# Optimization experiments

Measured on AMD Instinct MI355X. Metric: run time of the kernel, lower is better.

## Reference

```python
import jax, jax.numpy as jnp
import numpy as np

H = 512  # hidden_size; feature dim is 2H = 1024


def setup_inputs() -> dict:
    key = jax.random.key(0)
    ks = jax.random.split(key, 8)
    B, S, D2 = 32, 2048, 2 * H
    scale = 1.0 / np.sqrt(D2)
    return {
        "query": jax.random.normal(ks[0], (B, 4, H), dtype=jnp.float32),
        "keys": jax.random.normal(ks[1], (B, S, D2), dtype=jnp.float32),
        "Wa_w": jax.random.uniform(ks[2], (D2, D2), jnp.float32, -scale, scale),
        "Wa_b": jax.random.uniform(ks[3], (D2,), jnp.float32, -scale, scale),
        "Ua_w": jax.random.uniform(ks[4], (D2, D2), jnp.float32, -scale, scale),
        "Ua_b": jax.random.uniform(ks[5], (D2,), jnp.float32, -scale, scale),
        "Va_w": jax.random.uniform(ks[6], (1, D2), jnp.float32, -scale, scale),
        "Va_b": jax.random.uniform(ks[7], (1,), jnp.float32, -scale, scale),
    }


def reference(query, keys, Wa_w, Wa_b, Ua_w, Ua_b, Va_w, Va_b):
    B, D = query.shape[0], query.shape[-1]
    q = query.reshape(B, 2, -1, D)
    # last timestep of each direction, concatenated -> (B, 1, 2H)
    q = jnp.concatenate([q[:, 0, -1, :], q[:, 1, -1, :]], axis=-1)[:, None, :]
    # additive attention energies: (B, S, 2H)
    e = jnp.tanh((q @ Wa_w.T + Wa_b) + (keys @ Ua_w.T + Ua_b))
    scores = (e @ Va_w.T + Va_b)[..., 0][:, None, :]  # (B, 1, S)
    weights = jax.nn.softmax(scores, axis=-1)
    context = jnp.einsum("bqs,bsd->bqd", weights, keys)  # (B, 1, 2H)
    return context, weights
```

## Files before the change

### kernel.cpp

```cpp
#include <hip/hip_runtime.h>
#include <hip/hip_bf16.h>


typedef __attribute__((ext_vector_type(8))) short bf16x8;
typedef __attribute__((ext_vector_type(4))) float f32x4;

__device__ __forceinline__ unsigned pk_bf16(float x, float y) {
  union { __hip_bfloat162 h; unsigned u; } c;
  c.h = __float22bfloat162_rn(make_float2(x, y));
  return c.u;
}

__device__ __forceinline__ float fast_tanh(float x) {
  float e = __expf(2.0f * x);
  return 1.0f - 2.0f / (e + 1.0f);
}

typedef const __attribute__((address_space(1))) void* gas_t;
typedef __attribute__((address_space(3))) void* las_t;
__device__ __forceinline__ void ld_lds16(const void* g, void* l) {
  __builtin_amdgcn_global_load_lds((gas_t)g, (las_t)l, 16, 0, 0);
}

__global__ __launch_bounds__(256) void k_cvt_all(const float4* __restrict__ keys,
                                                 const float4* __restrict__ ua,
                                                 uint2* __restrict__ keys16,
                                                 uint2* __restrict__ ua16) {
  size_t i = (size_t)blockIdx.x * 256 + threadIdx.x;
  const float4* src;
  uint2* dst;
  size_t idx;
  if (i < 262144) { src = ua; dst = ua16; idx = i; }
  else            { src = keys; dst = keys16; idx = i - 262144; }
  float4 v = src[idx];
  uint2 o;
  o.x = pk_bf16(v.x, v.y);
  o.y = pk_bf16(v.z, v.w);
  dst[idx] = o;
}

__global__ __launch_bounds__(256) void k_qw(const float* __restrict__ query,
                                            const float* __restrict__ Wa_w,
                                            const float* __restrict__ Wa_b,
                                            const float* __restrict__ Ua_b,
                                            float* __restrict__ qW) {
  const int jc = blockIdx.x, b = blockIdx.y, t = threadIdx.x;
  __shared__ float4 qloc[256];
  {
    const float* base = (t < 128) ? (query + b * 2048 + 512) : (query + b * 2048 + 1536 - 512);
    qloc[t] = *(const float4*)(base + t * 4);
  }
  __syncthreads();
  const int jl = t >> 3, ks = t & 7;
  const int j = jc * 32 + jl;
  const float* wrow = Wa_w + j * 1024;
  float s = 0.f;
  #pragma unroll
  for (int i = 0; i < 32; ++i) {
    float4 wv = *(const float4*)(wrow + i * 32 + ks * 4);
    float4 q4 = qloc[i * 8 + ks];
    s += wv.x * q4.x + wv.y * q4.y + wv.z * q4.z + wv.w * q4.w;
  }
  s += __shfl_xor(s, 1);
  s += __shfl_xor(s, 2);
  s += __shfl_xor(s, 4);
  if (ks == 0) qW[b * 1024 + j] = s + Wa_b[j] + Ua_b[j];
}

__global__ __launch_bounds__(256) void k_score2(const unsigned short* __restrict__ keys16,
                                                const unsigned short* __restrict__ Uab,
                                                const float* __restrict__ qW,
                                                const float* __restrict__ Va,
                                                float* __restrict__ scores) {
  __shared__ __align__(16) unsigned short As[128 * 64];
  __shared__ __align__(16) unsigned short Bs[128 * 64];
  const int h = blockIdx.x;
  const int x = h & 7, g = h >> 3;
  const int jblk = g & 7;
  const int rblk = x + ((g >> 3) << 3);
  const int t = threadIdx.x;
  const int lane = t & 63, w = t >> 6;
  const int wm = w >> 1, wn = w & 1;
  const int l15 = lane & 15, quad = lane >> 4;
  const int row0 = rblk * 128, j0 = jblk * 128;
  const int lr = lane >> 3;
  const int sg = (lane & 7) ^ lr;

  f32x4 acc[4][4];
  #pragma unroll
  for (int i = 0; i < 4; i++)
    #pragma unroll
    for (int j = 0; j < 4; j++) acc[i][j] = (f32x4){0.f, 0.f, 0.f, 0.f};

  const int rb = l15 & 7;
  const int aoff = (wm * 64 + l15) * 64;
  const int boff = (wn * 64 + l15) * 64;

  const unsigned short* ga = keys16 + (size_t)(row0 + (w * 4) * 8 + lr) * 1024 + sg * 8;
  const unsigned short* gb = Uab + (size_t)(j0 + (w * 4) * 8 + lr) * 1024 + sg * 8;

  for (int k0 = 0; k0 < 1024; k0 += 64) {
    if (k0) __syncthreads();
    #pragma unroll
    for (int i = 0; i < 4; ++i) {
      const int c = w * 4 + i;
      ld_lds16(ga + (size_t)i * 8 * 1024 + k0, As + c * 512);
      ld_lds16(gb + (size_t)i * 8 * 1024 + k0, Bs + c * 512);
    }
    __syncthreads();
    #pragma unroll
    for (int ks = 0; ks < 2; ++ks) {
      const int xf = ((ks * 4 + quad) ^ rb) * 8;
      bf16x8 af[4], bfr[4];
      #pragma unroll
      for (int i = 0; i < 4; i++) af[i] = *(const bf16x8*)(As + aoff + i * 1024 + xf);
      #pragma unroll
      for (int i = 0; i < 4; i++) bfr[i] = *(const bf16x8*)(Bs + boff + i * 1024 + xf);
      #pragma unroll
      for (int i = 0; i < 4; i++)
        #pragma unroll
        for (int j = 0; j < 4; j++)
          acc[i][j] = __builtin_amdgcn_mfma_f32_16x16x32_bf16(af[i], bfr[j], acc[i][j], 0, 0, 0);
    }
  }

  const int b = row0 >> 11;
  float va[4], qb[4];
  #pragma unroll
  for (int j = 0; j < 4; j++) {
    int jg = j0 + wn * 64 + j * 16 + l15;
    va[j] = Va[jg];
    qb[j] = qW[b * 1024 + jg];
  }
  #pragma unroll
  for (int i = 0; i < 4; i++) {
    #pragma unroll
    for (int r = 0; r < 4; r++) {
      float s = 0.f;
      #pragma unroll
      for (int j = 0; j < 4; j++)
        s += va[j] * fast_tanh(acc[i][j][r] + qb[j]);
      s += __shfl_xor(s, 1);
      s += __shfl_xor(s, 2);
      s += __shfl_xor(s, 4);
      s += __shfl_xor(s, 8);
      if (l15 == 0) {
        int rg = row0 + wm * 64 + i * 16 + quad * 4 + r;
        atomicAdd(&scores[rg], s);
      }
    }
  }
}

__global__ __launch_bounds__(256) void k_score1(const float* __restrict__ keys,
                                                const unsigned short* __restrict__ Uab,
                                                const float* __restrict__ qW,
                                                const float* __restrict__ Va,
                                                float* __restrict__ scores) {
  __shared__ __align__(16) unsigned short As[128 * 72];
  __shared__ __align__(16) unsigned short Bs[128 * 72];
  const int jblk = blockIdx.x, rblk = blockIdx.y;
  const int t = threadIdx.x;
  const int lane = t & 63, w = t >> 6;
  const int wm = w >> 1, wn = w & 1;
  const int l15 = lane & 15, quad = lane >> 4;
  const int row0 = rblk * 128, j0 = jblk * 128;
  f32x4 acc[4][4];
  #pragma unroll
  for (int i = 0; i < 4; i++)
    #pragma unroll
    for (int j = 0; j < 4; j++) acc[i][j] = (f32x4){0.f, 0.f, 0.f, 0.f};
  for (int k0 = 0; k0 < 1024; k0 += 64) {
    __syncthreads();
    #pragma unroll
    for (int i = 0; i < 8; ++i) {
      int c = i * 256 + t, m = c >> 4, f4 = c & 15;
      float4 v = *(const float4*)(keys + (size_t)(row0 + m) * 1024 + k0 + f4 * 4);
      uint2 p;
      p.x = pk_bf16(v.x, v.y);
      p.y = pk_bf16(v.z, v.w);
      *(uint2*)(As + m * 72 + f4 * 4) = p;
    }
    #pragma unroll
    for (int i = 0; i < 4; ++i) {
      int c = i * 256 + t, j = c >> 3, k8 = c & 7;
      *(uint4*)(Bs + j * 72 + k8 * 8) = *(const uint4*)(Uab + (size_t)(j0 + j) * 1024 + k0 + k8 * 8);
    }
    __syncthreads();
    #pragma unroll
    for (int ks = 0; ks < 2; ++ks) {
      bf16x8 af[4], bfr[4];
      #pragma unroll
      for (int i = 0; i < 4; i++)
        af[i] = *(const bf16x8*)(As + (wm * 64 + i * 16 + l15) * 72 + ks * 32 + quad * 8);
      #pragma unroll
      for (int i = 0; i < 4; i++)
        bfr[i] = *(const bf16x8*)(Bs + (wn * 64 + i * 16 + l15) * 72 + ks * 32 + quad * 8);
      #pragma unroll
      for (int i = 0; i < 4; i++)
        #pragma unroll
        for (int j = 0; j < 4; j++)
          acc[i][j] = __builtin_amdgcn_mfma_f32_16x16x32_bf16(af[i], bfr[j], acc[i][j], 0, 0, 0);
    }
  }
  const int b = row0 >> 11;
  float va[4], qb[4];
  #pragma unroll
  for (int j = 0; j < 4; j++) {
    int jg = j0 + wn * 64 + j * 16 + l15;
    va[j] = Va[jg];
    qb[j] = qW[b * 1024 + jg];
  }
  #pragma unroll
  for (int i = 0; i < 4; i++)
    #pragma unroll
    for (int r = 0; r < 4; r++) {
      float s = 0.f;
      #pragma unroll
      for (int j = 0; j < 4; j++) s += va[j] * fast_tanh(acc[i][j][r] + qb[j]);
      s += __shfl_xor(s, 1);
      s += __shfl_xor(s, 2);
      s += __shfl_xor(s, 4);
      s += __shfl_xor(s, 8);
      if (l15 == 0) atomicAdd(&scores[row0 + wm * 64 + i * 16 + quad * 4 + r], s);
    }
}

__global__ __launch_bounds__(256) void k_softmax(const float* __restrict__ scores,
                                                 float* __restrict__ wout,
                                                 float* __restrict__ ctx) {
  const int b = blockIdx.x, t = threadIdx.x;
  const int lane = t & 63, w = t >> 6;
  *(float4*)(ctx + b * 1024 + t * 4) = (float4){0.f, 0.f, 0.f, 0.f};
  __shared__ float red[4];
  float v[8];
  float mx = -1e30f;
  #pragma unroll
  for (int i = 0; i < 8; i++) {
    v[i] = scores[b * 2048 + i * 256 + t];
    mx = fmaxf(mx, v[i]);
  }
  #pragma unroll
  for (int off = 1; off < 64; off <<= 1) mx = fmaxf(mx, __shfl_xor(mx, off));
  if (lane == 0) red[w] = mx;
  __syncthreads();
  mx = fmaxf(fmaxf(red[0], red[1]), fmaxf(red[2], red[3]));
  float sum = 0.f;
  #pragma unroll
  for (int i = 0; i < 8; i++) {
    v[i] = __expf(v[i] - mx);
    sum += v[i];
  }
  #pragma unroll
  for (int off = 1; off < 64; off <<= 1) sum += __shfl_xor(sum, off);
  __syncthreads();
  if (lane == 0) red[w] = sum;
  __syncthreads();
  sum = red[0] + red[1] + red[2] + red[3];
  float inv = 1.0f / sum;
  #pragma unroll
  for (int i = 0; i < 8; i++) wout[b * 2048 + i * 256 + t] = v[i] * inv;
}

__global__ __launch_bounds__(256) void k_context(const float* __restrict__ keys,
                                                 const float* __restrict__ wts,
                                                 float* __restrict__ ctx) {
  const int sc = blockIdx.x;
  const int b  = blockIdx.y;
  const int t  = threadIdx.x;
  __shared__ float wl[64];
  if (t < 64) wl[t] = wts[b * 2048 + sc * 64 + t];
  __syncthreads();
  const float4* kp = (const float4*)(keys + ((size_t)(b * 2048 + sc * 64) << 10)) + t;
  float4 a = {0.f, 0.f, 0.f, 0.f};
  #pragma unroll 8
  for (int s = 0; s < 64; ++s) {
    float4 kv = kp[s * 256];
    float wv = wl[s];
    a.x += wv * kv.x; a.y += wv * kv.y; a.z += wv * kv.z; a.w += wv * kv.w;
  }
  float* o = ctx + b * 1024 + t * 4;
  atomicAdd(o + 0, a.x);
  atomicAdd(o + 1, a.y);
  atomicAdd(o + 2, a.z);
  atomicAdd(o + 3, a.w);
}

extern "C" void kernel_launch(void* const* d_in, const int* in_sizes, int n_in,
                              void* d_out, int out_size, void* d_ws, size_t ws_size,
                              hipStream_t stream) {
  const float* query = (const float*)d_in[0];
  const float* keys  = (const float*)d_in[1];
  const float* Wa_w  = (const float*)d_in[2];
  const float* Wa_b  = (const float*)d_in[3];
  const float* Ua_w  = (const float*)d_in[4];
  const float* Ua_b  = (const float*)d_in[5];
  const float* Va_w  = (const float*)d_in[6];

  float* scores = (float*)d_ws;
  float* qW     = scores + 65536;
  unsigned short* Uab    = (unsigned short*)(qW + 32768);
  unsigned short* keys16 = Uab + 1024 * 1024;
  const size_t NEED_A = 2490368ull + 134217728ull;

  float* ctx = (float*)d_out;
  float* wts = ctx + 32768;

  hipMemsetAsync(scores, 0, 65536 * sizeof(float), stream);
  k_qw<<<dim3(32, 32), 256, 0, stream>>>(query, Wa_w, Wa_b, Ua_b, qW);

  if (ws_size >= NEED_A) {
    k_cvt_all<<<66560, 256, 0, stream>>>((const float4*)keys, (const float4*)Ua_w,
                                         (uint2*)keys16, (uint2*)Uab);
    k_score2<<<4096, 256, 0, stream>>>(keys16, Uab, qW, Va_w, scores);
  } else {
    k_cvt_all<<<1024, 256, 0, stream>>>((const float4*)keys, (const float4*)Ua_w,
                                        (uint2*)keys16, (uint2*)Uab);
    k_score1<<<dim3(8, 512), 256, 0, stream>>>(keys, Uab, qW, Va_w, scores);
  }

  k_softmax<<<32, 256, 0, stream>>>(scores, wts, ctx);
  k_context<<<dim3(32, 32), 256, 0, stream>>>(keys, wts, ctx);
}
```

Baseline: 591.9 us.

## Fuse prologue kernels and compute context from bf16 keys

Merges the scores memset, the query projection and the fp32-to-bf16 conversion into one launch to cut launch overhead. The context reduction now reads the bf16 copy of keys instead of fp32, halving the bytes read in that stage, and splits rows across two half-blocks with an LDS combine. The score GEMM gets an occupancy hint and a reordered fragment load loop to lower register pressure. Using bf16 keys for the context reduces output precision.

```diff
diff --git a/kernel.cpp b/kernel.cpp
--- a/kernel.cpp
+++ b/kernel.cpp
@@ -11,6 +11,12 @@
   return c.u;
 }
 
+__device__ __forceinline__ float bf2f(short u) {
+  union { unsigned u; float f; } c;
+  c.u = ((unsigned)(unsigned short)u) << 16;
+  return c.f;
+}
+
 __device__ __forceinline__ float fast_tanh(float x) {
   float e = __expf(2.0f * x);
   return 1.0f - 2.0f / (e + 1.0f);
@@ -22,29 +28,33 @@
   __builtin_amdgcn_global_load_lds((gas_t)g, (las_t)l, 16, 0, 0);
 }
 
-__global__ __launch_bounds__(256) void k_cvt_all(const float4* __restrict__ keys,
-                                                 const float4* __restrict__ ua,
-                                                 uint2* __restrict__ keys16,
-                                                 uint2* __restrict__ ua16) {
-  size_t i = (size_t)blockIdx.x * 256 + threadIdx.x;
-  const float4* src;
-  uint2* dst;
-  size_t idx;
-  if (i < 262144) { src = ua; dst = ua16; idx = i; }
-  else            { src = keys; dst = keys16; idx = i - 262144; }
-  float4 v = src[idx];
-  uint2 o;
-  o.x = pk_bf16(v.x, v.y);
-  o.y = pk_bf16(v.z, v.w);
-  dst[idx] = o;
-}
-
-__global__ __launch_bounds__(256) void k_qw(const float* __restrict__ query,
-                                            const float* __restrict__ Wa_w,
-                                            const float* __restrict__ Wa_b,
-                                            const float* __restrict__ Ua_b,
-                                            float* __restrict__ qW) {
-  const int jc = blockIdx.x, b = blockIdx.y, t = threadIdx.x;
+__global__ __launch_bounds__(256) void k_fused(const float* __restrict__ query,
+                                               const float* __restrict__ Wa_w,
+                                               const float* __restrict__ Wa_b,
+                                               const float* __restrict__ Ua_b,
+                                               const float4* __restrict__ keys,
+                                               const float4* __restrict__ ua,
+                                               float* __restrict__ qW,
+                                               uint2* __restrict__ keys16,
+                                               uint2* __restrict__ ua16,
+                                               float* __restrict__ scores) {
+  const int t = threadIdx.x;
+  if (blockIdx.x >= 1024) {
+    size_t i = (size_t)(blockIdx.x - 1024) * 256 + t;
+    const float4* src;
+    uint2* dst;
+    size_t idx;
+    if (i < 262144) { src = ua; dst = ua16; idx = i; }
+    else            { src = keys; dst = keys16; idx = i - 262144; }
+    float4 v = src[idx];
+    uint2 o;
+    o.x = pk_bf16(v.x, v.y);
+    o.y = pk_bf16(v.z, v.w);
+    dst[idx] = o;
+    return;
+  }
+  if (t < 64) scores[blockIdx.x * 64 + t] = 0.f;
+  const int jc = blockIdx.x >> 5, b = blockIdx.x & 31;
   __shared__ float4 qloc[256];
   {
     const float* base = (t < 128) ? (query + b * 2048 + 512) : (query + b * 2048 + 1536 - 512);
@@ -67,11 +77,11 @@
   if (ks == 0) qW[b * 1024 + j] = s + Wa_b[j] + Ua_b[j];
 }
 
-__global__ __launch_bounds__(256) void k_score2(const unsigned short* __restrict__ keys16,
-                                                const unsigned short* __restrict__ Uab,
-                                                const float* __restrict__ qW,
-                                                const float* __restrict__ Va,
-                                                float* __restrict__ scores) {
+__global__ __launch_bounds__(256, 4) void k_score2(const unsigned short* __restrict__ keys16,
+                                                   const unsigned short* __restrict__ Uab,
+                                                   const float* __restrict__ qW,
+                                                   const float* __restrict__ Va,
+                                                   float* __restrict__ scores) {
   __shared__ __align__(16) unsigned short As[128 * 64];
   __shared__ __align__(16) unsigned short Bs[128 * 64];
   const int h = blockIdx.x;
@@ -111,16 +121,18 @@
     #pragma unroll
     for (int ks = 0; ks < 2; ++ks) {
       const int xf = ((ks * 4 + quad) ^ rb) * 8;
-      bf16x8 af[4], bfr[4];
-      #pragma unroll
-      for (int i = 0; i < 4; i++) af[i] = *(const bf16x8*)(As + aoff + i * 1024 + xf);
-      #pragma unroll
-      for (int i = 0; i < 4; i++) bfr[i] = *(const bf16x8*)(Bs + boff + i * 1024 + xf);
-      #pragma unroll
-      for (int i = 0; i < 4; i++)
-        #pragma unroll
-        for (int j = 0; j < 4; j++)
-          acc[i][j] = __builtin_amdgcn_mfma_f32_16x16x32_bf16(af[i], bfr[j], acc[i][j], 0, 0, 0);
+      bf16x8 bfr0 = *(const bf16x8*)(Bs + boff + 0 * 1024 + xf);
+      bf16x8 bfr1 = *(const bf16x8*)(Bs + boff + 1 * 1024 + xf);
+      bf16x8 bfr2 = *(const bf16x8*)(Bs + boff + 2 * 1024 + xf);
+      bf16x8 bfr3 = *(const bf16x8*)(Bs + boff + 3 * 1024 + xf);
+      #pragma unroll
+      for (int i = 0; i < 4; i++) {
+        bf16x8 af = *(const bf16x8*)(As + aoff + i * 1024 + xf);
+        acc[i][0] = __builtin_amdgcn_mfma_f32_16x16x32_bf16(af, bfr0, acc[i][0], 0, 0, 0);
+        acc[i][1] = __builtin_amdgcn_mfma_f32_16x16x32_bf16(af, bfr1, acc[i][1], 0, 0, 0);
+        acc[i][2] = __builtin_amdgcn_mfma_f32_16x16x32_bf16(af, bfr2, acc[i][2], 0, 0, 0);
+        acc[i][3] = __builtin_amdgcn_mfma_f32_16x16x32_bf16(af, bfr3, acc[i][3], 0, 0, 0);
+      }
     }
   }
 
@@ -262,9 +274,41 @@
   for (int i = 0; i < 8; i++) wout[b * 2048 + i * 256 + t] = v[i] * inv;
 }
 
-__global__ __launch_bounds__(256) void k_context(const float* __restrict__ keys,
-                                                 const float* __restrict__ wts,
-                                                 float* __restrict__ ctx) {
+__global__ __launch_bounds__(256) void k_context2(const unsigned short* __restrict__ keys16,
+                                                  const float* __restrict__ wts,
+                                                  float* __restrict__ ctx) {
+  const int sc = blockIdx.x;
+  const int b  = blockIdx.y;
+  const int t  = threadIdx.x;
+  const int so = t >> 7, tc = t & 127;
+  __shared__ float wl[64];
+  __shared__ float ps[128 * 8];
+  if (t < 64) wl[t] = wts[b * 2048 + sc * 64 + t];
+  __syncthreads();
+  const unsigned short* kp = keys16 + (size_t)(b * 2048 + sc * 64 + so) * 1024 + tc * 8;
+  float a[8] = {0.f, 0.f, 0.f, 0.f, 0.f, 0.f, 0.f, 0.f};
+  #pragma unroll 4
+  for (int s = 0; s < 64; s += 2) {
+    bf16x8 kv = *(const bf16x8*)(kp + (size_t)s * 1024);
+    float wv = wl[s + so];
+    #pragma unroll
+    for (int i = 0; i < 8; i++) a[i] += wv * bf2f(kv[i]);
+  }
+  if (so == 1) {
+    #pragma unroll
+    for (int i = 0; i < 8; i++) ps[tc * 8 + i] = a[i];
+  }
+  __syncthreads();
+  if (so == 0) {
+    float* o = ctx + b * 1024 + tc * 8;
+    #pragma unroll
+    for (int i = 0; i < 8; i++) atomicAdd(o + i, a[i] + ps[tc * 8 + i]);
+  }
+}
+
+__global__ __launch_bounds__(256) void k_context1(const float* __restrict__ keys,
+                                                  const float* __restrict__ wts,
+                                                  float* __restrict__ ctx) {
   const int sc = blockIdx.x;
   const int b  = blockIdx.y;
   const int t  = threadIdx.x;
@@ -306,19 +350,19 @@
   float* ctx = (float*)d_out;
   float* wts = ctx + 32768;
 
-  hipMemsetAsync(scores, 0, 65536 * sizeof(float), stream);
-  k_qw<<<dim3(32, 32), 256, 0, stream>>>(query, Wa_w, Wa_b, Ua_b, qW);
-
   if (ws_size >= NEED_A) {
-    k_cvt_all<<<66560, 256, 0, stream>>>((const float4*)keys, (const float4*)Ua_w,
-                                         (uint2*)keys16, (uint2*)Uab);
+    k_fused<<<67584, 256, 0, stream>>>(query, Wa_w, Wa_b, Ua_b, (const float4*)keys,
+                                       (const float4*)Ua_w, qW, (uint2*)keys16,
+                                       (uint2*)Uab, scores);
     k_score2<<<4096, 256, 0, stream>>>(keys16, Uab, qW, Va_w, scores);
+    k_softmax<<<32, 256, 0, stream>>>(scores, wts, ctx);
+    k_context2<<<dim3(32, 32), 256, 0, stream>>>(keys16, wts, ctx);
   } else {
-    k_cvt_all<<<1024, 256, 0, stream>>>((const float4*)keys, (const float4*)Ua_w,
-                                        (uint2*)keys16, (uint2*)Uab);
+    k_fused<<<2048, 256, 0, stream>>>(query, Wa_w, Wa_b, Ua_b, (const float4*)keys,
+                                      (const float4*)Ua_w, qW, (uint2*)keys16,
+                                      (uint2*)Uab, scores);
     k_score1<<<dim3(8, 512), 256, 0, stream>>>(keys, Uab, qW, Va_w, scores);
-  }
-
-  k_softmax<<<32, 256, 0, stream>>>(scores, wts, ctx);
-  k_context<<<dim3(32, 32), 256, 0, stream>>>(keys, wts, ctx);
-}
+    k_softmax<<<32, 256, 0, stream>>>(scores, wts, ctx);
+    k_context1<<<dim3(32, 32), 256, 0, stream>>>(keys, wts, ctx);
+  }
+}
```

Result: faster. 578.3 us (-2.3%).
